# Optimization experiments

Hardware: AMD Instinct MI355X
Metric: run time of the kernel (lower is better)

## Reference

```python
import jax, jax.numpy as jnp
import numpy as np

N_NODES = 100000
N_EDGES = 1200000
IN_DIM, HID, OUT = 128, 64, 64


def setup_inputs() -> dict:
    key = jax.random.key(0)
    ks = jax.random.split(key, 16)
    s = 0.05
    return {
        "x": jax.random.normal(ks[0], (N_NODES, IN_DIM), jnp.float32),
        "fc_w": jax.random.normal(ks[1], (IN_DIM, HID), jnp.float32) * s,
        "fc_b": jnp.zeros((HID,), jnp.float32),
        "conv1_w": jax.random.normal(ks[2], (IN_DIM, HID), jnp.float32) * s,
        "conv1_b": jnp.zeros((HID,), jnp.float32),
        "fc1_w": jax.random.normal(ks[3], (2 * HID, OUT), jnp.float32) * s,
        "fc1_b": jnp.zeros((OUT,), jnp.float32),
        "conv2_w": jax.random.normal(ks[4], (2 * HID, OUT), jnp.float32) * s,
        "conv2_b": jnp.zeros((OUT,), jnp.float32),
        "fc2_w": jax.random.normal(ks[5], (OUT, 1), jnp.float32) * s,
        "fc2_b": jnp.zeros((1,), jnp.float32),
        "conv3_w": jax.random.normal(ks[6], (OUT, 1), jnp.float32) * s,
        "conv3_b": jnp.zeros((1,), jnp.float32),
        "edge_index": jax.random.randint(ks[7], (2, N_EDGES), 0, N_NODES, jnp.int64 if jax.config.jax_enable_x64 else jnp.int32),
    }


def gcn_conv(h_in, w, b, row, col, norm, n_nodes):
    # PyG GCNConv (no self loops): scatter_add(norm * (XW)[row]) at col, + bias
    h = h_in @ w                                  # [N, F_out]
    msg = h[row] * norm[:, None]                  # [E, F_out]
    out = jax.ops.segment_sum(msg, col, num_segments=n_nodes)
    return out + b


def reference(x, fc_w, fc_b, conv1_w, conv1_b, fc1_w, fc1_b, conv2_w, conv2_b,
              fc2_w, fc2_b, conv3_w, conv3_b, edge_index):
    n = x.shape[0]
    row, col = edge_index[0], edge_index[1]
    # symmetric normalization: deg over destination nodes (unit edge weights)
    deg = jax.ops.segment_sum(jnp.ones(row.shape[0], x.dtype), col, num_segments=n)
    dinv = jnp.where(deg > 0, jax.lax.rsqrt(jnp.maximum(deg, 1.0)), 0.0)
    norm = dinv[row] * dinv[col]                  # [E]

    x1 = jax.nn.relu(x @ fc_w + fc_b)             # MLP branch [N, HID]
    x2 = jax.nn.relu(gcn_conv(x, conv1_w, conv1_b, row, col, norm, n))
    x3 = jnp.concatenate([x1, x2], axis=1)        # [N, 2*HID]
    x5 = jax.nn.relu(x3 @ fc1_w + fc1_b)
    x6 = jax.nn.relu(gcn_conv(x3, conv2_w, conv2_b, row, col, norm, n))
    x7 = x5 + x6                                  # residual combine [N, OUT]
    x9 = x7 @ fc2_w + fc2_b
    x10 = gcn_conv(x7, conv3_w, conv3_b, row, col, norm, n)
    return x9 + x10                               # [N, 1]
```

## Files before the change

kernel.cpp:

```cpp
#include <hip/hip_runtime.h>

#define IN_DIM 128
#define HID 64
#define RB_SHIFT 10
#define RB 1024
#define NBMAX 128
#define MAXBIN 16384
#define PCH 2048

typedef short bf16x8 __attribute__((ext_vector_type(8)));
typedef float f32x4  __attribute__((ext_vector_type(4)));

__device__ __forceinline__ float relu(float v) { return v > 0.f ? v : 0.f; }

__device__ __forceinline__ unsigned short f2bf(float f) {
    unsigned u = __float_as_uint(f);
    u += 0x7FFFu + ((u >> 16) & 1u);
    return (unsigned short)(u >> 16);
}
__device__ __forceinline__ float bflo(unsigned u) { return __uint_as_float(u << 16); }
__device__ __forceinline__ float bfhi(unsigned u) { return __uint_as_float(u & 0xFFFF0000u); }

__global__ __launch_bounds__(256) void k_wprep(const float* __restrict__ W1a,
                                               const float* __restrict__ W2a,
                                               const float* __restrict__ W1b,
                                               const float* __restrict__ W2b,
                                               unsigned short* __restrict__ Wt,
                                               int* __restrict__ binCursor, int NR) {
    if (blockIdx.x == 0 && threadIdx.x < NR) binCursor[threadIdx.x] = threadIdx.x * MAXBIN;
    const int t = blockIdx.x * 256 + threadIdx.x;
    if (t >= 2 * 4 * 8 * 64) return;
    const int lane = t & 63;
    const int c = (t >> 6) & 7;
    const int kc = (t >> 9) & 3;
    const int layer = t >> 11;
    const int col = c * 16 + (lane & 15);
    const int k0 = kc * 32 + (lane >> 4) * 8;
    const float* W1 = layer ? W1b : W1a;
    const float* W2 = layer ? W2b : W2a;
    const float* src = (col < 64) ? (W1 + col) : (W2 + (col - 64));
    unsigned short v[8];
#pragma unroll
    for (int j = 0; j < 8; j++) v[j] = f2bf(src[(size_t)(k0 + j) * 64]);
    *(ushort4*)(Wt + (size_t)t * 8) = make_ushort4(v[0], v[1], v[2], v[3]);
    *(ushort4*)(Wt + (size_t)t * 8 + 4) = make_ushort4(v[4], v[5], v[6], v[7]);
}

__global__ __launch_bounds__(256) void k_part(const int* __restrict__ row,
                                              const int* __restrict__ col,
                                              int* __restrict__ binCursor,
                                              int2* __restrict__ part, int E) {
    __shared__ int lcur[NBMAX], gbase[NBMAX];
    const int tid = threadIdx.x;
    const int e0 = blockIdx.x * PCH;
    const int cnt = min(PCH, E - e0);
    if (tid < NBMAX) lcur[tid] = 0;
    __syncthreads();
    int rr[8], cc[8], pp[8];
    if (cnt == PCH) {
#pragma unroll
        for (int h = 0; h < 2; h++) {
            const int4 c4 = *(const int4*)(col + e0 + h * 1024 + tid * 4);
            const int4 r4 = *(const int4*)(row + e0 + h * 1024 + tid * 4);
            cc[h * 4 + 0] = c4.x; cc[h * 4 + 1] = c4.y;
            cc[h * 4 + 2] = c4.z; cc[h * 4 + 3] = c4.w;
            rr[h * 4 + 0] = r4.x; rr[h * 4 + 1] = r4.y;
            rr[h * 4 + 2] = r4.z; rr[h * 4 + 3] = r4.w;
        }
    } else {
#pragma unroll
        for (int j = 0; j < 8; j++) {
            const int e = e0 + j * 256 + tid;
            if (e < e0 + cnt) { rr[j] = row[e]; cc[j] = col[e]; }
            else cc[j] = -1;
        }
    }
#pragma unroll
    for (int j = 0; j < 8; j++)
        if (cc[j] >= 0) pp[j] = atomicAdd(&lcur[cc[j] >> RB_SHIFT], 1);
    __syncthreads();
    if (tid < NBMAX && lcur[tid] > 0)
        gbase[tid] = atomicAdd(&binCursor[tid], lcur[tid]);
    __syncthreads();
#pragma unroll
    for (int j = 0; j < 8; j++)
        if (cc[j] >= 0)
            part[gbase[cc[j] >> RB_SHIFT] + pp[j]] = make_int2(rr[j], cc[j]);
}

__global__ __launch_bounds__(256) void k_csr(const int* __restrict__ binCursor,
                                             const int2* __restrict__ part,
                                             int* __restrict__ degi,
                                             float* __restrict__ dinv,
                                             int* __restrict__ start,
                                             int* __restrict__ rs, int N) {
    __shared__ int cnt[RB];
    __shared__ int psum[256];
    const int b = blockIdx.x;
    const int lo = b << RB_SHIFT;
    const int tid = threadIdx.x;
    for (int i = tid; i < RB; i += 256) cnt[i] = 0;
    __syncthreads();
    const int base = b * MAXBIN;
    const int tot = binCursor[b] - base;
    for (int i = tid; i < tot; i += 256)
        atomicAdd(&cnt[part[base + i].y - lo], 1);
    __syncthreads();
    const int i0 = tid * 4;
    const int c0 = cnt[i0], c1 = cnt[i0 + 1], c2 = cnt[i0 + 2], c3 = cnt[i0 + 3];
    const int s = c0 + c1 + c2 + c3;
    psum[tid] = s;
    __syncthreads();
    for (int off = 1; off < 256; off <<= 1) {
        int t = (tid >= off) ? psum[tid - off] : 0;
        __syncthreads();
        psum[tid] += t;
        __syncthreads();
    }
    const int e = psum[tid] - s;
    const int offs[4] = {e, e + c0, e + c0 + c1, e + c0 + c1 + c2};
    const int cs[4] = {c0, c1, c2, c3};
#pragma unroll
    for (int j = 0; j < 4; j++) {
        const int n = lo + i0 + j;
        if (n < N) {
            degi[n] = cs[j];
            start[n] = base + offs[j];
            dinv[n] = cs[j] > 0 ? rsqrtf((float)cs[j]) : 0.f;
        }
        cnt[i0 + j] = base + offs[j];
    }
    __syncthreads();
    for (int i = tid; i < tot; i += 256) {
        const int2 v = part[base + i];
        const int pos = atomicAdd(&cnt[v.y - lo], 1);
        rs[pos] = v.x;
    }
}

template <int LAYER>
__global__ __launch_bounds__(256) void k_gemm(const float* __restrict__ XF,
                                              const unsigned short* __restrict__ X1B,
                                              const unsigned short* __restrict__ X2B,
                                              const unsigned short* __restrict__ Wt,
                                              const float* __restrict__ B1,
                                              const float* __restrict__ dinv,
                                              float* __restrict__ O1f,
                                              unsigned short* __restrict__ O1b,
                                              unsigned short* __restrict__ O2,
                                              int N) {
    const int tid = threadIdx.x;
    const int wave = tid >> 6;
    const int lane = tid & 63;
    const int quad = lane >> 4;
    const int lm = lane & 15;
    const int n0 = blockIdx.x * 64 + wave * 16;
    if (n0 >= N) return;
    const int nrow = min(n0 + lm, N - 1);

    f32x4 acc[8];
#pragma unroll
    for (int c = 0; c < 8; c++) acc[c] = (f32x4){0.f, 0.f, 0.f, 0.f};

#pragma unroll
    for (int kc = 0; kc < 4; kc++) {
        const int k0 = kc * 32 + quad * 8;
        bf16x8 a;
        if (LAYER == 1) {
            const float* s = XF + (size_t)nrow * IN_DIM + k0;
            const float4 q0 = *(const float4*)s;
            const float4 q1 = *(const float4*)(s + 4);
            a[0] = (short)f2bf(q0.x); a[1] = (short)f2bf(q0.y);
            a[2] = (short)f2bf(q0.z); a[3] = (short)f2bf(q0.w);
            a[4] = (short)f2bf(q1.x); a[5] = (short)f2bf(q1.y);
            a[6] = (short)f2bf(q1.z); a[7] = (short)f2bf(q1.w);
        } else {
            const unsigned short* s = (kc < 2) ? (X1B + (size_t)nrow * 64 + k0)
                                               : (X2B + (size_t)nrow * 64 + (k0 - 64));
            a = *(const bf16x8*)s;
        }
#pragma unroll
        for (int c = 0; c < 8; c++) {
            const bf16x8 b = *(const bf16x8*)(Wt + (size_t)((kc * 8 + c) * 64 + lane) * 8);
            acc[c] = __builtin_amdgcn_mfma_f32_16x16x32_bf16(a, b, acc[c], 0, 0, 0);
        }
    }

    const int nb = n0 + quad * 4;
    float dvv[4];
#pragma unroll
    for (int r = 0; r < 4; r++) dvv[r] = (nb + r < N) ? dinv[nb + r] : 0.f;
#pragma unroll
    for (int c = 0; c < 4; c++) {
        const int col = c * 16 + lm;
        const float b = B1[col];
#pragma unroll
        for (int r = 0; r < 4; r++) {
            const int n = nb + r;
            if (n < N) {
                const float v = relu(acc[c][r] + b);
                if (LAYER == 1) O1b[(size_t)n * 64 + col] = f2bf(v);
                else            O1f[(size_t)n * 64 + col] = v;
            }
        }
    }
#pragma unroll
    for (int c = 4; c < 8; c++) {
        const int col = (c - 4) * 16 + lm;
#pragma unroll
        for (int r = 0; r < 4; r++) {
            const int n = nb + r;
            if (n < N) O2[(size_t)n * 64 + col] = f2bf(acc[c][r] * dvv[r]);
        }
    }
}

template <int MODE>
__global__ __launch_bounds__(256) void k_gather(const int* __restrict__ start,
                                                const int* __restrict__ degi,
                                                const int* __restrict__ rs,
                                                const unsigned short* __restrict__ H,
                                                const float* __restrict__ dinv,
                                                const float* __restrict__ CB,
                                                unsigned short* __restrict__ OXB,
                                                const float* __restrict__ X5,
                                                const float* __restrict__ FC2W,
                                                const float* __restrict__ FC2B,
                                                const float* __restrict__ C3W,
                                                const float* __restrict__ C3B,
                                                float* __restrict__ H3,
                                                float* __restrict__ OUT, int N) {
    const int l = threadIdx.x & 7;
    const int d = blockIdx.x * 32 + (threadIdx.x >> 3);
    if (d >= N) return;
    int s = start[d];
    const int e2 = s + degi[d];
    float a0 = 0.f, a1 = 0.f, a2 = 0.f, a3 = 0.f;
    float a4 = 0.f, a5 = 0.f, a6 = 0.f, a7 = 0.f;
#define ACC8(u)                                                          \
    a0 += bflo(u.x); a1 += bfhi(u.x); a2 += bflo(u.y); a3 += bfhi(u.y);  \
    a4 += bflo(u.z); a5 += bfhi(u.z); a6 += bflo(u.w); a7 += bfhi(u.w);
    for (; s + 3 < e2; s += 4) {
        const int4 e4 = *(const int4*)(rs + s);
        const uint4 ua = *(const uint4*)(H + (size_t)e4.x * 64 + l * 8);
        const uint4 ub = *(const uint4*)(H + (size_t)e4.y * 64 + l * 8);
        const uint4 uc = *(const uint4*)(H + (size_t)e4.z * 64 + l * 8);
        const uint4 ud = *(const uint4*)(H + (size_t)e4.w * 64 + l * 8);
        ACC8(ua) ACC8(ub) ACC8(uc) ACC8(ud)
    }
    for (; s < e2; ++s) {
        const uint4 ua = *(const uint4*)(H + (size_t)rs[s] * 64 + l * 8);
        ACC8(ua)
    }
#undef ACC8
    const float dd = dinv[d];
    const float4 cba = *(const float4*)(CB + l * 8);
    const float4 cbb = *(const float4*)(CB + l * 8 + 4);
    const float r0 = relu(dd * a0 + cba.x), r1 = relu(dd * a1 + cba.y);
    const float r2 = relu(dd * a2 + cba.z), r3 = relu(dd * a3 + cba.w);
    const float r4 = relu(dd * a4 + cbb.x), r5 = relu(dd * a5 + cbb.y);
    const float r6 = relu(dd * a6 + cbb.z), r7 = relu(dd * a7 + cbb.w);
    if (MODE == 1) {
        uint4 o;
        o.x = (unsigned)f2bf(r0) | ((unsigned)f2bf(r1) << 16);
        o.y = (unsigned)f2bf(r2) | ((unsigned)f2bf(r3) << 16);
        o.z = (unsigned)f2bf(r4) | ((unsigned)f2bf(r5) << 16);
        o.w = (unsigned)f2bf(r6) | ((unsigned)f2bf(r7) << 16);
        *(uint4*)(OXB + (size_t)d * 64 + l * 8) = o;
    } else {
        const float4 xa = *(const float4*)(X5 + (size_t)d * 64 + l * 8);
        const float4 xb = *(const float4*)(X5 + (size_t)d * 64 + l * 8 + 4);
        const float v0 = xa.x + r0, v1 = xa.y + r1, v2 = xa.z + r2, v3 = xa.w + r3;
        const float v4 = xb.x + r4, v5 = xb.y + r5, v6 = xb.z + r6, v7 = xb.w + r7;
        const float4 w9a = *(const float4*)(FC2W + l * 8);
        const float4 w9b = *(const float4*)(FC2W + l * 8 + 4);
        const float4 wXa = *(const float4*)(C3W + l * 8);
        const float4 wXb = *(const float4*)(C3W + l * 8 + 4);
        float p9 = v0 * w9a.x + v1 * w9a.y + v2 * w9a.z + v3 * w9a.w
                 + v4 * w9b.x + v5 * w9b.y + v6 * w9b.z + v7 * w9b.w;
        float p10 = v0 * wXa.x + v1 * wXa.y + v2 * wXa.z + v3 * wXa.w
                  + v4 * wXb.x + v5 * wXb.y + v6 * wXb.z + v7 * wXb.w;
#pragma unroll
        for (int m = 1; m < 8; m <<= 1) {
            p9 += __shfl_xor(p9, m, 64);
            p10 += __shfl_xor(p10, m, 64);
        }
        if (l == 0) {
            OUT[d] = p9 + FC2B[0] + C3B[0];
            H3[d] = p10 * dd;
        }
    }
}

__global__ __launch_bounds__(256) void k_gather1f(const int* __restrict__ start,
                                                  const int* __restrict__ degi,
                                                  const int* __restrict__ rs,
                                                  const float* __restrict__ H3,
                                                  const float* __restrict__ dinv,
                                                  float* __restrict__ OUT, int N) {
    const int d = blockIdx.x * 256 + threadIdx.x;
    if (d >= N) return;
    int s = start[d];
    const int e2 = s + degi[d];
    float acc = 0.f;
    for (; s + 3 < e2; s += 4) {
        const int4 e4 = *(const int4*)(rs + s);
        acc += H3[e4.x] + H3[e4.y] + H3[e4.z] + H3[e4.w];
    }
    for (; s < e2; ++s) acc += H3[rs[s]];
    OUT[d] += acc * dinv[d];
}

extern "C" void kernel_launch(void* const* d_in, const int* in_sizes, int n_in,
                              void* d_out, int out_size, void* d_ws, size_t ws_size,
                              hipStream_t stream) {
    const float* x    = (const float*)d_in[0];
    const float* fcw  = (const float*)d_in[1];
    const float* fcb  = (const float*)d_in[2];
    const float* c1w  = (const float*)d_in[3];
    const float* c1b  = (const float*)d_in[4];
    const float* f1w  = (const float*)d_in[5];
    const float* f1b  = (const float*)d_in[6];
    const float* c2w  = (const float*)d_in[7];
    const float* c2b  = (const float*)d_in[8];
    const float* f2w  = (const float*)d_in[9];
    const float* f2b  = (const float*)d_in[10];
    const float* c3w  = (const float*)d_in[11];
    const float* c3b  = (const float*)d_in[12];
    const int*   ei   = (const int*)d_in[13];

    const int N = in_sizes[0] / IN_DIM;
    const int E = in_sizes[13] / 2;
    const int* row = ei;
    const int* col = ei + E;
    float* out = (float*)d_out;

    const int NR = (N + RB - 1) >> RB_SHIFT;

    const size_t Npad = ((size_t)N + 127) & ~(size_t)127;
    const size_t NF = (size_t)N * 64;
    const size_t REG = (size_t)NR * MAXBIN;
    int*   binCur = (int*)d_ws;
    int*   degi   = binCur + NBMAX;
    float* dinv   = (float*)(degi + Npad);
    int*   start  = (int*)(dinv + Npad);
    unsigned short* Wt = (unsigned short*)(start + Npad);
    int2*  part   = (int2*)(Wt + 2 * 16384);
    int*   rs     = (int*)(part + REG);
    unsigned short* x1bf = (unsigned short*)(rs + REG);
    unsigned short* h1   = x1bf + NF;
    unsigned short* x2bf = h1 + NF;
    float* x5     = (float*)(x2bf + NF);
    float* h3     = x5 + NF;
    unsigned short* h2 = h1;

    const int gN = (N + 255) / 256;
    const int gG = (N + 63) / 64;
    const int gW = (N + 31) / 32;
    const int gP = (E + PCH - 1) / PCH;

    k_wprep<<<16, 256, 0, stream>>>(fcw, c1w, f1w, c2w, Wt, binCur, NR);
    k_part<<<gP, 256, 0, stream>>>(row, col, binCur, part, E);
    k_csr<<<NR, 256, 0, stream>>>(binCur, part, degi, dinv, start, rs, N);

    k_gemm<1><<<gG, 256, 0, stream>>>(x, nullptr, nullptr, Wt, fcb, dinv,
                                      nullptr, x1bf, h1, N);
    k_gather<1><<<gW, 256, 0, stream>>>(start, degi, rs, h1, dinv, c1b, x2bf,
                                        nullptr, nullptr, nullptr, nullptr,
                                        nullptr, nullptr, nullptr, N);

    k_gemm<2><<<gG, 256, 0, stream>>>(nullptr, x1bf, x2bf, Wt + 16384, f1b, dinv,
                                      x5, nullptr, h2, N);
    k_gather<2><<<gW, 256, 0, stream>>>(start, degi, rs, h2, dinv, c2b, nullptr,
                                        x5, f2w, f2b, c3w, c3b, h3, out, N);
    k_gather1f<<<gN, 256, 0, stream>>>(start, degi, rs, h3, dinv, out, N);
}
```

Baseline: 260.2 us.

## Fuse first-layer gather with second GEMM, pack edge partition, store x5 as bf16

The layer-1 neighbour aggregation now feeds straight into the layer-2 MFMA GEMM inside one kernel. The aggregated x2 tile stays in shared memory instead of going to global memory and being read back, and one launch is removed. The edge partition buffer packs source and destination-low-bits into a single int instead of an int2, which halves that scatter traffic. x5 is stored as bf16 rather than fp32, cutting its write and read bandwidth at some precision cost. The fused kernel uses 32-node blocks with waves split across output columns, which gives less MFMA work per wave and may lower GEMM efficiency. Packing assumes node ids fit in 22 bits.

```diff
diff --git a/kernel.cpp b/kernel.cpp
--- a/kernel.cpp
+++ b/kernel.cpp
@@ -1,7 +1,6 @@
 #include <hip/hip_runtime.h>
 
 #define IN_DIM 128
-#define HID 64
 #define RB_SHIFT 10
 #define RB 1024
 #define NBMAX 128
@@ -49,7 +48,7 @@
 __global__ __launch_bounds__(256) void k_part(const int* __restrict__ row,
                                               const int* __restrict__ col,
                                               int* __restrict__ binCursor,
-                                              int2* __restrict__ part, int E) {
+                                              int* __restrict__ part, int E) {
     __shared__ int lcur[NBMAX], gbase[NBMAX];
     const int tid = threadIdx.x;
     const int e0 = blockIdx.x * PCH;
@@ -85,11 +84,12 @@
 #pragma unroll
     for (int j = 0; j < 8; j++)
         if (cc[j] >= 0)
-            part[gbase[cc[j] >> RB_SHIFT] + pp[j]] = make_int2(rr[j], cc[j]);
+            part[gbase[cc[j] >> RB_SHIFT] + pp[j]] =
+                (rr[j] << RB_SHIFT) | (cc[j] & (RB - 1));
 }
 
 __global__ __launch_bounds__(256) void k_csr(const int* __restrict__ binCursor,
-                                             const int2* __restrict__ part,
+                                             const int* __restrict__ part,
                                              int* __restrict__ degi,
                                              float* __restrict__ dinv,
                                              int* __restrict__ start,
@@ -104,7 +104,7 @@
     const int base = b * MAXBIN;
     const int tot = binCursor[b] - base;
     for (int i = tid; i < tot; i += 256)
-        atomicAdd(&cnt[part[base + i].y - lo], 1);
+        atomicAdd(&cnt[part[base + i] & (RB - 1)], 1);
     __syncthreads();
     const int i0 = tid * 4;
     const int c0 = cnt[i0], c1 = cnt[i0 + 1], c2 = cnt[i0 + 2], c3 = cnt[i0 + 3];
@@ -132,23 +132,19 @@
     }
     __syncthreads();
     for (int i = tid; i < tot; i += 256) {
-        const int2 v = part[base + i];
-        const int pos = atomicAdd(&cnt[v.y - lo], 1);
-        rs[pos] = v.x;
-    }
-}
-
-template <int LAYER>
-__global__ __launch_bounds__(256) void k_gemm(const float* __restrict__ XF,
-                                              const unsigned short* __restrict__ X1B,
-                                              const unsigned short* __restrict__ X2B,
-                                              const unsigned short* __restrict__ Wt,
-                                              const float* __restrict__ B1,
-                                              const float* __restrict__ dinv,
-                                              float* __restrict__ O1f,
-                                              unsigned short* __restrict__ O1b,
-                                              unsigned short* __restrict__ O2,
-                                              int N) {
+        const int v = part[base + i];
+        const int pos = atomicAdd(&cnt[v & (RB - 1)], 1);
+        rs[pos] = v >> RB_SHIFT;
+    }
+}
+
+__global__ __launch_bounds__(256) void k_gemm1(const float* __restrict__ XF,
+                                               const unsigned short* __restrict__ Wt,
+                                               const float* __restrict__ B1,
+                                               const float* __restrict__ dinv,
+                                               unsigned short* __restrict__ O1b,
+                                               unsigned short* __restrict__ O2,
+                                               int N) {
     const int tid = threadIdx.x;
     const int wave = tid >> 6;
     const int lane = tid & 63;
@@ -165,20 +161,14 @@
 #pragma unroll
     for (int kc = 0; kc < 4; kc++) {
         const int k0 = kc * 32 + quad * 8;
+        const float* s = XF + (size_t)nrow * IN_DIM + k0;
+        const float4 q0 = *(const float4*)s;
+        const float4 q1 = *(const float4*)(s + 4);
         bf16x8 a;
-        if (LAYER == 1) {
-            const float* s = XF + (size_t)nrow * IN_DIM + k0;
-            const float4 q0 = *(const float4*)s;
-            const float4 q1 = *(const float4*)(s + 4);
-            a[0] = (short)f2bf(q0.x); a[1] = (short)f2bf(q0.y);
-            a[2] = (short)f2bf(q0.z); a[3] = (short)f2bf(q0.w);
-            a[4] = (short)f2bf(q1.x); a[5] = (short)f2bf(q1.y);
-            a[6] = (short)f2bf(q1.z); a[7] = (short)f2bf(q1.w);
-        } else {
-            const unsigned short* s = (kc < 2) ? (X1B + (size_t)nrow * 64 + k0)
-                                               : (X2B + (size_t)nrow * 64 + (k0 - 64));
-            a = *(const bf16x8*)s;
-        }
+        a[0] = (short)f2bf(q0.x); a[1] = (short)f2bf(q0.y);
+        a[2] = (short)f2bf(q0.z); a[3] = (short)f2bf(q0.w);
+        a[4] = (short)f2bf(q1.x); a[5] = (short)f2bf(q1.y);
+        a[6] = (short)f2bf(q1.z); a[7] = (short)f2bf(q1.w);
 #pragma unroll
         for (int c = 0; c < 8; c++) {
             const bf16x8 b = *(const bf16x8*)(Wt + (size_t)((kc * 8 + c) * 64 + lane) * 8);
@@ -197,11 +187,7 @@
 #pragma unroll
         for (int r = 0; r < 4; r++) {
             const int n = nb + r;
-            if (n < N) {
-                const float v = relu(acc[c][r] + b);
-                if (LAYER == 1) O1b[(size_t)n * 64 + col] = f2bf(v);
-                else            O1f[(size_t)n * 64 + col] = v;
-            }
+            if (n < N) O1b[(size_t)n * 64 + col] = f2bf(relu(acc[c][r] + b));
         }
     }
 #pragma unroll
@@ -215,21 +201,130 @@
     }
 }
 
-template <int MODE>
-__global__ __launch_bounds__(256) void k_gather(const int* __restrict__ start,
-                                                const int* __restrict__ degi,
-                                                const int* __restrict__ rs,
-                                                const unsigned short* __restrict__ H,
-                                                const float* __restrict__ dinv,
-                                                const float* __restrict__ CB,
-                                                unsigned short* __restrict__ OXB,
-                                                const float* __restrict__ X5,
-                                                const float* __restrict__ FC2W,
-                                                const float* __restrict__ FC2B,
-                                                const float* __restrict__ C3W,
-                                                const float* __restrict__ C3B,
-                                                float* __restrict__ H3,
-                                                float* __restrict__ OUT, int N) {
+#define ACC8(u)                                                          \
+    a0 += bflo(u.x); a1 += bfhi(u.x); a2 += bflo(u.y); a3 += bfhi(u.y);  \
+    a4 += bflo(u.z); a5 += bfhi(u.z); a6 += bflo(u.w); a7 += bfhi(u.w);
+
+__global__ __launch_bounds__(256) void k_gfuse(const int* __restrict__ start,
+                                               const int* __restrict__ degi,
+                                               const int* __restrict__ rs,
+                                               const unsigned short* __restrict__ H,
+                                               const float* __restrict__ dinv,
+                                               const float* __restrict__ CB,
+                                               const unsigned short* __restrict__ X1B,
+                                               const unsigned short* __restrict__ Wt,
+                                               const float* __restrict__ B1,
+                                               unsigned short* __restrict__ X5B,
+                                               unsigned short* __restrict__ H2,
+                                               int N) {
+    __shared__ __align__(16) unsigned short x2s[32][72];
+    const int tid = threadIdx.x;
+    const int l = tid & 7;
+    const int di = tid >> 3;
+    const int d = blockIdx.x * 32 + di;
+
+    uint4 ov = make_uint4(0u, 0u, 0u, 0u);
+    if (d < N) {
+        int s = start[d];
+        const int e2 = s + degi[d];
+        float a0 = 0.f, a1 = 0.f, a2 = 0.f, a3 = 0.f;
+        float a4 = 0.f, a5 = 0.f, a6 = 0.f, a7 = 0.f;
+        for (; s + 3 < e2; s += 4) {
+            const int4 e4 = *(const int4*)(rs + s);
+            const uint4 ua = *(const uint4*)(H + (size_t)e4.x * 64 + l * 8);
+            const uint4 ub = *(const uint4*)(H + (size_t)e4.y * 64 + l * 8);
+            const uint4 uc = *(const uint4*)(H + (size_t)e4.z * 64 + l * 8);
+            const uint4 ud = *(const uint4*)(H + (size_t)e4.w * 64 + l * 8);
+            ACC8(ua) ACC8(ub) ACC8(uc) ACC8(ud)
+        }
+        for (; s < e2; ++s) {
+            const uint4 ua = *(const uint4*)(H + (size_t)rs[s] * 64 + l * 8);
+            ACC8(ua)
+        }
+        const float dd = dinv[d];
+        const float4 cba = *(const float4*)(CB + l * 8);
+        const float4 cbb = *(const float4*)(CB + l * 8 + 4);
+        ov.x = (unsigned)f2bf(relu(dd * a0 + cba.x)) |
+               ((unsigned)f2bf(relu(dd * a1 + cba.y)) << 16);
+        ov.y = (unsigned)f2bf(relu(dd * a2 + cba.z)) |
+               ((unsigned)f2bf(relu(dd * a3 + cba.w)) << 16);
+        ov.z = (unsigned)f2bf(relu(dd * a4 + cbb.x)) |
+               ((unsigned)f2bf(relu(dd * a5 + cbb.y)) << 16);
+        ov.w = (unsigned)f2bf(relu(dd * a6 + cbb.z)) |
+               ((unsigned)f2bf(relu(dd * a7 + cbb.w)) << 16);
+    }
+    *(uint4*)&x2s[di][l * 8] = ov;
+    __syncthreads();
+
+    const int wave = tid >> 6;
+    const int lane = tid & 63;
+    const int quad = lane >> 4;
+    const int lm = lane & 15;
+    const int nh = (wave >> 1) * 16;
+    const int cb4 = (wave & 1) * 4;
+    const int n0 = blockIdx.x * 32 + nh;
+    if (n0 >= N) return;
+    const int nrow = min(n0 + lm, N - 1);
+
+    f32x4 acc[4];
+#pragma unroll
+    for (int c = 0; c < 4; c++) acc[c] = (f32x4){0.f, 0.f, 0.f, 0.f};
+#pragma unroll
+    for (int kc = 0; kc < 4; kc++) {
+        bf16x8 a;
+        if (kc < 2) {
+            a = *(const bf16x8*)(X1B + (size_t)nrow * 64 + kc * 32 + quad * 8);
+        } else {
+            a = *(const bf16x8*)&x2s[nh + lm][(kc - 2) * 32 + quad * 8];
+        }
+#pragma unroll
+        for (int c = 0; c < 4; c++) {
+            const bf16x8 b =
+                *(const bf16x8*)(Wt + (size_t)((kc * 8 + cb4 + c) * 64 + lane) * 8);
+            acc[c] = __builtin_amdgcn_mfma_f32_16x16x32_bf16(a, b, acc[c], 0, 0, 0);
+        }
+    }
+    const int nb = n0 + quad * 4;
+    if (cb4 == 0) {
+#pragma unroll
+        for (int c = 0; c < 4; c++) {
+            const int col = c * 16 + lm;
+            const float b = B1[col];
+#pragma unroll
+            for (int r = 0; r < 4; r++) {
+                const int n = nb + r;
+                if (n < N) X5B[(size_t)n * 64 + col] = f2bf(relu(acc[c][r] + b));
+            }
+        }
+    } else {
+        float dvv[4];
+#pragma unroll
+        for (int r = 0; r < 4; r++) dvv[r] = (nb + r < N) ? dinv[nb + r] : 0.f;
+#pragma unroll
+        for (int c = 0; c < 4; c++) {
+            const int col = c * 16 + lm;
+#pragma unroll
+            for (int r = 0; r < 4; r++) {
+                const int n = nb + r;
+                if (n < N) H2[(size_t)n * 64 + col] = f2bf(acc[c][r] * dvv[r]);
+            }
+        }
+    }
+}
+
+__global__ __launch_bounds__(256) void k_gather2(const int* __restrict__ start,
+                                                 const int* __restrict__ degi,
+                                                 const int* __restrict__ rs,
+                                                 const unsigned short* __restrict__ H,
+                                                 const float* __restrict__ dinv,
+                                                 const float* __restrict__ CB,
+                                                 const unsigned short* __restrict__ X5B,
+                                                 const float* __restrict__ FC2W,
+                                                 const float* __restrict__ FC2B,
+                                                 const float* __restrict__ C3W,
+                                                 const float* __restrict__ C3B,
+                                                 float* __restrict__ H3,
+                                                 float* __restrict__ OUT, int N) {
     const int l = threadIdx.x & 7;
     const int d = blockIdx.x * 32 + (threadIdx.x >> 3);
     if (d >= N) return;
@@ -237,9 +332,6 @@
     const int e2 = s + degi[d];
     float a0 = 0.f, a1 = 0.f, a2 = 0.f, a3 = 0.f;
     float a4 = 0.f, a5 = 0.f, a6 = 0.f, a7 = 0.f;
-#define ACC8(u)                                                          \
-    a0 += bflo(u.x); a1 += bfhi(u.x); a2 += bflo(u.y); a3 += bfhi(u.y);  \
-    a4 += bflo(u.z); a5 += bfhi(u.z); a6 += bflo(u.w); a7 += bfhi(u.w);
     for (; s + 3 < e2; s += 4) {
         const int4 e4 = *(const int4*)(rs + s);
         const uint4 ua = *(const uint4*)(H + (size_t)e4.x * 64 + l * 8);
@@ -252,45 +344,37 @@
         const uint4 ua = *(const uint4*)(H + (size_t)rs[s] * 64 + l * 8);
         ACC8(ua)
     }
-#undef ACC8
     const float dd = dinv[d];
     const float4 cba = *(const float4*)(CB + l * 8);
     const float4 cbb = *(const float4*)(CB + l * 8 + 4);
-    const float r0 = relu(dd * a0 + cba.x), r1 = relu(dd * a1 + cba.y);
-    const float r2 = relu(dd * a2 + cba.z), r3 = relu(dd * a3 + cba.w);
-    const float r4 = relu(dd * a4 + cbb.x), r5 = relu(dd * a5 + cbb.y);
-    const float r6 = relu(dd * a6 + cbb.z), r7 = relu(dd * a7 + cbb.w);
-    if (MODE == 1) {
-        uint4 o;
-        o.x = (unsigned)f2bf(r0) | ((unsigned)f2bf(r1) << 16);
-        o.y = (unsigned)f2bf(r2) | ((unsigned)f2bf(r3) << 16);
-        o.z = (unsigned)f2bf(r4) | ((unsigned)f2bf(r5) << 16);
-        o.w = (unsigned)f2bf(r6) | ((unsigned)f2bf(r7) << 16);
-        *(uint4*)(OXB + (size_t)d * 64 + l * 8) = o;
-    } else {
-        const float4 xa = *(const float4*)(X5 + (size_t)d * 64 + l * 8);
-        const float4 xb = *(const float4*)(X5 + (size_t)d * 64 + l * 8 + 4);
-        const float v0 = xa.x + r0, v1 = xa.y + r1, v2 = xa.z + r2, v3 = xa.w + r3;
-        const float v4 = xb.x + r4, v5 = xb.y + r5, v6 = xb.z + r6, v7 = xb.w + r7;
-        const float4 w9a = *(const float4*)(FC2W + l * 8);
-        const float4 w9b = *(const float4*)(FC2W + l * 8 + 4);
-        const float4 wXa = *(const float4*)(C3W + l * 8);
-        const float4 wXb = *(const float4*)(C3W + l * 8 + 4);
-        float p9 = v0 * w9a.x + v1 * w9a.y + v2 * w9a.z + v3 * w9a.w
-                 + v4 * w9b.x + v5 * w9b.y + v6 * w9b.z + v7 * w9b.w;
-        float p10 = v0 * wXa.x + v1 * wXa.y + v2 * wXa.z + v3 * wXa.w
-                  + v4 * wXb.x + v5 * wXb.y + v6 * wXb.z + v7 * wXb.w;
-#pragma unroll
-        for (int m = 1; m < 8; m <<= 1) {
-            p9 += __shfl_xor(p9, m, 64);
-            p10 += __shfl_xor(p10, m, 64);
-        }
-        if (l == 0) {
-            OUT[d] = p9 + FC2B[0] + C3B[0];
-            H3[d] = p10 * dd;
-        }
-    }
-}
+    const uint4 xv = *(const uint4*)(X5B + (size_t)d * 64 + l * 8);
+    const float v0 = bflo(xv.x) + relu(dd * a0 + cba.x);
+    const float v1 = bfhi(xv.x) + relu(dd * a1 + cba.y);
+    const float v2 = bflo(xv.y) + relu(dd * a2 + cba.z);
+    const float v3 = bfhi(xv.y) + relu(dd * a3 + cba.w);
+    const float v4 = bflo(xv.z) + relu(dd * a4 + cbb.x);
+    const float v5 = bfhi(xv.z) + relu(dd * a5 + cbb.y);
+    const float v6 = bflo(xv.w) + relu(dd * a6 + cbb.z);
+    const float v7 = bfhi(xv.w) + relu(dd * a7 + cbb.w);
+    const float4 w9a = *(const float4*)(FC2W + l * 8);
+    const float4 w9b = *(const float4*)(FC2W + l * 8 + 4);
+    const float4 wXa = *(const float4*)(C3W + l * 8);
+    const float4 wXb = *(const float4*)(C3W + l * 8 + 4);
+    float p9 = v0 * w9a.x + v1 * w9a.y + v2 * w9a.z + v3 * w9a.w
+             + v4 * w9b.x + v5 * w9b.y + v6 * w9b.z + v7 * w9b.w;
+    float p10 = v0 * wXa.x + v1 * wXa.y + v2 * wXa.z + v3 * wXa.w
+              + v4 * wXb.x + v5 * wXb.y + v6 * wXb.z + v7 * wXb.w;
+#pragma unroll
+    for (int m = 1; m < 8; m <<= 1) {
+        p9 += __shfl_xor(p9, m, 64);
+        p10 += __shfl_xor(p10, m, 64);
+    }
+    if (l == 0) {
+        OUT[d] = p9 + FC2B[0] + C3B[0];
+        H3[d] = p10 * dd;
+    }
+}
+#undef ACC8
 
 __global__ __launch_bounds__(256) void k_gather1f(const int* __restrict__ start,
                                                   const int* __restrict__ degi,
@@ -345,33 +429,29 @@
     float* dinv   = (float*)(degi + Npad);
     int*   start  = (int*)(dinv + Npad);
     unsigned short* Wt = (unsigned short*)(start + Npad);
-    int2*  part   = (int2*)(Wt + 2 * 16384);
-    int*   rs     = (int*)(part + REG);
+    int*   part   = (int*)(Wt + 2 * 16384);
+    int*   rs     = part + REG;
     unsigned short* x1bf = (unsigned short*)(rs + REG);
     unsigned short* h1   = x1bf + NF;
-    unsigned short* x2bf = h1 + NF;
-    float* x5     = (float*)(x2bf + NF);
-    float* h3     = x5 + NF;
-    unsigned short* h2 = h1;
+    unsigned short* h2   = h1 + NF;
+    unsigned short* x5b  = h2 + NF;
+    float* h3     = (float*)(x5b + NF);
 
     const int gN = (N + 255) / 256;
     const int gG = (N + 63) / 64;
-    const int gW = (N + 31) / 32;
+    const int gF = (N + 31) / 32;
     const int gP = (E + PCH - 1) / PCH;
 
     k_wprep<<<16, 256, 0, stream>>>(fcw, c1w, f1w, c2w, Wt, binCur, NR);
     k_part<<<gP, 256, 0, stream>>>(row, col, binCur, part, E);
     k_csr<<<NR, 256, 0, stream>>>(binCur, part, degi, dinv, start, rs, N);
 
-    k_gemm<1><<<gG, 256, 0, stream>>>(x, nullptr, nullptr, Wt, fcb, dinv,
-                                      nullptr, x1bf, h1, N);
-    k_gather<1><<<gW, 256, 0, stream>>>(start, degi, rs, h1, dinv, c1b, x2bf,
-                                        nullptr, nullptr, nullptr, nullptr,
-                                        nullptr, nullptr, nullptr, N);
-
-    k_gemm<2><<<gG, 256, 0, stream>>>(nullptr, x1bf, x2bf, Wt + 16384, f1b, dinv,
-                                      x5, nullptr, h2, N);
-    k_gather<2><<<gW, 256, 0, stream>>>(start, degi, rs, h2, dinv, c2b, nullptr,
-                                        x5, f2w, f2b, c3w, c3b, h3, out, N);
+    k_gemm1<<<gG, 256, 0, stream>>>(x, Wt, fcb, dinv, x1bf, h1, N);
+
+    k_gfuse<<<gF, 256, 0, stream>>>(start, degi, rs, h1, dinv, c1b,
+                                    x1bf, Wt + 16384, f1b, x5b, h2, N);
+
+    k_gather2<<<gF, 256, 0, stream>>>(start, degi, rs, h2, dinv, c2b, x5b,
+                                      f2w, f2b, c3w, c3b, h3, out, N);
     k_gather1f<<<gN, 256, 0, stream>>>(start, degi, rs, h3, dinv, out, N);
 }
```

New measurement: 252.4 us. 3.0% less time.
